# Kernel optimization log

Measured on AMD Instinct MI355X. Metric: run time of the kernel, lower is better.

The kernel has to match this reference:

```python
import jax, jax.numpy as jnp
import numpy as np

IMG = 416
NC = 80
B = 32
NOBJ = 20          # objects placed per image
K = 32             # fixed max GT boxes per image for ignore-mask IoU (>= NOBJ)
THR = 0.5
ANCHORS = np.array([[10,13],[16,30],[33,23],[30,61],[62,45],[59,119],
                    [116,90],[156,198],[373,326]], np.float32)


def _bce(logits, targets):
    # elementwise binary_cross_entropy_with_logits
    return jnp.maximum(logits, 0.0) - logits * targets + jnp.log1p(jnp.exp(-jnp.abs(logits)))


def _make_y_true(key, batch, G, nc, img, nobj):
    N = G * G * 3
    k1, k2, k3, k4 = jax.random.split(key, 4)
    idx = jax.random.randint(k1, (batch, nobj), 0, N)
    xy = jax.random.uniform(k2, (batch, nobj, 2), jnp.float32) * img
    wh = jax.random.uniform(k3, (batch, nobj, 2), jnp.float32) * 90.0 + 10.0
    cls = jax.random.randint(k4, (batch, nobj), 0, nc)
    y = jnp.zeros((batch, N, 5 + nc), jnp.float32)
    b = jnp.arange(batch)[:, None]
    y = y.at[b, idx, 0].set(xy[..., 0])
    y = y.at[b, idx, 1].set(xy[..., 1])
    y = y.at[b, idx, 2].set(wh[..., 0])
    y = y.at[b, idx, 3].set(wh[..., 1])
    y = y.at[b, idx, 4].set(1.0)
    y = y.at[b, idx, 5 + cls].set(1.0)
    return y.reshape(batch, G, G, 3, 5 + nc)


def setup_inputs() -> dict:
    key = jax.random.key(0)
    ks = jax.random.split(key, 6)
    inp = {}
    for i, G in enumerate([13, 26, 52]):
        inp[f"fm{i}"] = jax.random.normal(ks[i], (B, 3 * (5 + NC), G, G), jnp.float32)
        inp[f"yt{i}"] = _make_y_true(ks[3 + i], B, G, NC, IMG, NOBJ)
    inp["anchors"] = jnp.asarray(ANCHORS)
    return inp


def _predict_transform(fm, anchors3):
    batch, ch, G, _ = fm.shape
    A = 3
    stride = IMG // G
    bbox = 5 + NC
    # [B, A*bbox, G*G] -> [B, G*G, A*bbox] -> [B, G, G, A, bbox]
    p = fm.reshape(batch, A * bbox, G * G).transpose(0, 2, 1).reshape(batch, G, G, A, bbox)
    box_centers = jax.nn.sigmoid(p[..., 0:2])
    box_sizes_raw = p[..., 2:4]
    conf_logits = p[..., 4:5]
    prob_logits = p[..., 5:]
    ar = jnp.arange(G, dtype=fm.dtype)
    gy, gx = jnp.meshgrid(ar, ar, indexing='ij')       # row, col
    xy_offset = jnp.stack([gx, gy], axis=-1).reshape(G, G, 1, 2)
    box_centers = (box_centers + xy_offset) * stride
    box_sizes = jnp.exp(box_sizes_raw) * (anchors3 / stride) * stride
    boxes = jnp.concatenate([box_centers, box_sizes], axis=-1)
    return xy_offset, boxes, conf_logits, prob_logits


def _ignore_mask(boxes, yt):
    batch, G, _, A, _ = boxes.shape
    N = G * G * A
    pb = boxes.reshape(batch, N, 4)
    tb_all = yt[..., :4].reshape(batch, N, 4)
    obj = yt[..., 4].reshape(batch, N)
    vals, idx = jax.lax.top_k(obj, K)                  # pick up to K GT boxes
    valid = vals > 0                                    # [B,K]
    tb = jnp.take_along_axis(tb_all, idx[:, :, None], axis=1)  # [B,K,4]
    tb = jnp.where(valid[:, :, None], tb, 0.0)
    p_xy = pb[:, :, None, 0:2]; p_wh = pb[:, :, None, 2:4]     # [B,N,1,2]
    t_xy = tb[:, None, :, 0:2]; t_wh = tb[:, None, :, 2:4]     # [B,1,K,2]
    mins = jnp.maximum(p_xy - p_wh / 2.0, t_xy - t_wh / 2.0)
    maxs = jnp.minimum(p_xy + p_wh / 2.0, t_xy + t_wh / 2.0)
    iwh = jnp.maximum(maxs - mins, 0.0)
    inter = iwh[..., 0] * iwh[..., 1]                  # [B,N,K]
    p_area = p_wh[..., 0] * p_wh[..., 1]
    t_area = t_wh[..., 0] * t_wh[..., 1]
    iou = inter / (p_area + t_area - inter + 1e-10)
    iou = jnp.where(valid[:, None, :], iou, 0.0)
    best_iou = jnp.max(iou, axis=-1)                   # [B,N]
    ign = (best_iou < THR).astype(boxes.dtype)
    # original: images with no valid GT boxes keep ignore_mask = 0
    ign = jnp.where(jnp.any(valid, axis=-1)[:, None], ign, 0.0)
    return ign.reshape(batch, G, G, A, 1)


def _calculate_one(fm, yt, anchors3):
    G = fm.shape[2]
    batch = yt.shape[0]
    ratio = IMG / G
    xy_offset, boxes, conf_logits, prob_logits = _predict_transform(fm, anchors3)
    object_mask = yt[..., 4:5]
    ignore_mask = _ignore_mask(boxes, yt)
    true_xy = yt[..., 0:2] / ratio - xy_offset
    pred_xy = boxes[..., 0:2] / ratio - xy_offset
    true_tw = yt[..., 2:4] / anchors3
    pred_tw = boxes[..., 2:4] / anchors3
    true_tw = jnp.where(true_tw == 0.0, 1.0, true_tw)
    pred_tw = jnp.where(pred_tw == 0.0, 1.0, pred_tw)
    true_tw = jnp.log(jnp.clip(true_tw, 1e-9, 1e9))
    pred_tw = jnp.log(jnp.clip(pred_tw, 1e-9, 1e9))
    box_scale = 2.0 - (yt[..., 2:3] / IMG) * (yt[..., 3:4] / IMG)
    xy_loss = 5.0 * jnp.sum((true_xy - pred_xy) ** 2 * object_mask * box_scale) / batch
    wh_loss = 5.0 * jnp.sum((true_tw - pred_tw) ** 2 * object_mask * box_scale) / batch
    bce_conf = _bce(conf_logits, object_mask)
    conf_loss = object_mask * bce_conf + 0.5 * (1.0 - object_mask) * ignore_mask * bce_conf
    focal = jnp.abs(object_mask - jax.nn.sigmoid(conf_logits)) ** 2.0   # alpha=1, gamma=2
    conf_loss = jnp.sum(conf_loss * focal) / batch
    delta = 0.01
    label_target = (1.0 - delta) * yt[..., 5:] + delta / NC
    class_loss = jnp.sum(object_mask * _bce(prob_logits, label_target)) / batch
    return xy_loss, wh_loss, conf_loss, class_loss


def reference(fm0, fm1, fm2, yt0, yt1, yt2, anchors):
    anchor_groups = [anchors[6:9], anchors[3:6], anchors[0:3]]
    fms = [fm0, fm1, fm2]
    yts = [yt0, yt1, yt2]
    xy = wh = conf = prob = 0.0
    for fm, yt, a3 in zip(fms, yts, anchor_groups):
        l_xy, l_wh, l_conf, l_prob = _calculate_one(fm, yt, a3)
        xy = xy + l_xy; wh = wh + l_wh; conf = conf + l_conf; prob = prob + l_prob
    total = xy + wh + conf + prob
    return (total, xy, wh, conf, prob)
```

## Files before the change

kernel.cpp:

```cpp
#include <hip/hip_runtime.h>
#include <math.h>


constexpr int   NCLS  = 80;
constexpr int   KMAX  = 32;
constexpr float IMGF  = 416.0f;

constexpr int C0 = 32 * 3 * 169;
constexpr int C1 = 32 * 3 * 676;
constexpr int C2 = 32 * 3 * 2704;
constexpr int TOTAL_CELLS = C0 + C1 + C2;

constexpr int NBLK_POS  = 96;
constexpr int NBLK_CONF = 96 + 288 + 1056;
constexpr int NBLK_MAIN = NBLK_POS + NBLK_CONF;

constexpr size_t OFF_PART = 0;
constexpr size_t OFF_CNT  = (size_t)NBLK_MAIN * 16;
constexpr size_t OFF_TGT  = OFF_CNT + 96 * sizeof(int);
constexpr size_t OFF_TGTN = OFF_TGT + (size_t)96 * KMAX * 16;

__global__ __launch_bounds__(128) void k_init(int* cnt) {
    int t = threadIdx.x;
    if (t < 96) cnt[t] = 0;
}

__global__ __launch_bounds__(256) void k_collect(
        const float* __restrict__ yt0, const float* __restrict__ yt1,
        const float* __restrict__ yt2,
        int* __restrict__ cnt, float* __restrict__ tgt, int* __restrict__ tgtn) {
    int t = blockIdx.x * 256 + threadIdx.x;
    if (t >= TOTAL_CELLS) return;
    int s, local, G;
    const float* yt;
    if (t < C0)           { s = 0; local = t;           G = 13; yt = yt0; }
    else if (t < C0 + C1) { s = 1; local = t - C0;      G = 26; yt = yt1; }
    else                  { s = 2; local = t - C0 - C1; G = 52; yt = yt2; }
    int GG = G * G;
    int b  = local / (3 * GG);
    int n  = local - b * 3 * GG;
    int yidx = local * 85;
    float obj = yt[yidx + 4];
    if (obj > 0.5f) {
        int pos = atomicAdd(&cnt[s * 32 + b], 1);
        if (pos < KMAX) {
            float4 box = make_float4(yt[yidx], yt[yidx + 1], yt[yidx + 2], yt[yidx + 3]);
            reinterpret_cast<float4*>(tgt)[(s * 32 + b) * KMAX + pos] = box;
            tgtn[(s * 32 + b) * KMAX + pos] = n;
        }
    }
}

__device__ inline float sigmoidf_(float x) { return 1.0f / (1.0f + expf(-x)); }
__device__ inline float bcef_(float l, float t) {
    return fmaxf(l, 0.0f) - l * t + log1pf(expf(-fabsf(l)));
}

__global__ __launch_bounds__(256) void k_main(
        const float* __restrict__ fm0, const float* __restrict__ fm1,
        const float* __restrict__ fm2,
        const float* __restrict__ yt0, const float* __restrict__ yt1,
        const float* __restrict__ yt2,
        const float* __restrict__ anch,
        const int* __restrict__ cnt, const float* __restrict__ tgt,
        const int* __restrict__ tgtn, float4* __restrict__ part) {
    __shared__ float s_minx[KMAX], s_maxx[KMAX], s_miny[KMAX], s_maxy[KMAX], s_area[KMAX];
    __shared__ int   s_tn[KMAX];
    __shared__ int   s_cn;
    __shared__ float4 s_w4[4];
    __shared__ float  s_w1[4];

    int bid = blockIdx.x;
    int tid = threadIdx.x;
    int wid = tid >> 6, lane = tid & 63;

    if (bid < NBLK_POS) {
        int sb = bid, s = sb >> 5, b = sb & 31;
        const float *fm, *yt;
        int G, anchoff;
        if (s == 0)      { fm = fm0; yt = yt0; G = 13; anchoff = 6; }
        else if (s == 1) { fm = fm1; yt = yt1; G = 26; anchoff = 3; }
        else             { fm = fm2; yt = yt2; G = 52; anchoff = 0; }
        int GG = G * G;
        float stridef = IMGF / (float)G;
        int cn = min(cnt[sb], KMAX);
        float accx = 0.f, accw = 0.f, accp = 0.f;
        for (int slot = wid; slot < cn; slot += 4) {
            float4 tb = reinterpret_cast<const float4*>(tgt)[sb * KMAX + slot];
            int n  = tgtn[sb * KMAX + slot];
            int a  = n % 3;
            int sp = n / 3;
            int jj = sp % G, ii = sp / G;
            int ybase = (b * 3 * GG + n) * 85;
            int fbase = (b * 255 + a * 85) * GG + sp;
            float ps = 0.0f;
            for (int c = lane; c < NCLS; c += 64) {
                float pl  = fm[fbase + (5 + c) * GG];
                float tl  = yt[ybase + 5 + c];
                float lab = 0.99f * tl + 1.25e-4f;
                ps += bcef_(pl, lab);
            }
            for (int off = 32; off; off >>= 1) ps += __shfl_down(ps, off);
            if (lane == 0) {
                float p0 = fm[fbase];
                float p1 = fm[fbase + GG];
                float p2 = fm[fbase + 2 * GG];
                float p3 = fm[fbase + 3 * GG];
                float bcx = (sigmoidf_(p0) + (float)jj) * stridef;
                float bcy = (sigmoidf_(p1) + (float)ii) * stridef;
                float predx = bcx / stridef - (float)jj;
                float predy = bcy / stridef - (float)ii;
                float truex = tb.x / stridef - (float)jj;
                float truey = tb.y / stridef - (float)ii;
                float dx = truex - predx, dy = truey - predy;
                float bscale = 2.0f - (tb.z / IMGF) * (tb.w / IMGF);
                float aw = anch[(anchoff + a) * 2], ah = anch[(anchoff + a) * 2 + 1];
                float pw = expf(p2) * (aw / stridef) * stridef;
                float ph = expf(p3) * (ah / stridef) * stridef;
                float ptw = pw / aw, pth = ph / ah;
                float ttw = tb.z / aw, tth = tb.w / ah;
                ttw = (ttw == 0.0f) ? 1.0f : ttw;
                tth = (tth == 0.0f) ? 1.0f : tth;
                ptw = (ptw == 0.0f) ? 1.0f : ptw;
                pth = (pth == 0.0f) ? 1.0f : pth;
                ttw = logf(fminf(fmaxf(ttw, 1e-9f), 1e9f));
                tth = logf(fminf(fmaxf(tth, 1e-9f), 1e9f));
                ptw = logf(fminf(fmaxf(ptw, 1e-9f), 1e9f));
                pth = logf(fminf(fmaxf(pth, 1e-9f), 1e9f));
                float dw = ttw - ptw, dh = tth - pth;
                accx += (dx * dx + dy * dy) * bscale;
                accw += (dw * dw + dh * dh) * bscale;
                accp += ps;
            }
        }
        if (lane == 0) s_w4[wid] = make_float4(accx, accw, accp, 0.f);
        __syncthreads();
        if (tid == 0) {
            float4 r0 = s_w4[0], r1 = s_w4[1], r2 = s_w4[2], r3 = s_w4[3];
            part[bid] = make_float4(r0.x + r1.x + r2.x + r3.x,
                                    r0.y + r1.y + r2.y + r3.y,
                                    r0.z + r1.z + r2.z + r3.z,
                                    0.0f);
        }
    } else {
        int cb = bid - NBLK_POS;
        const float *fm;
        int G, chunks, s, anchoff;
        if (cb < 96)       { fm = fm0; G = 13; chunks = 1;  s = 0; anchoff = 6; }
        else if (cb < 384) { cb -= 96;  fm = fm1; G = 26; chunks = 3;  s = 1; anchoff = 3; }
        else               { cb -= 384; fm = fm2; G = 52; chunks = 11; s = 2; anchoff = 0; }
        int chunk = cb % chunks;
        int ba    = cb / chunks;
        int b = ba / 3, a = ba % 3;
        int GG = G * G;
        float stridef = IMGF / (float)G;
        int sb = s * 32 + b;

        if (tid == 0) s_cn = min(cnt[sb], KMAX);
        if (tid < KMAX) {
            float4 tb = reinterpret_cast<const float4*>(tgt)[sb * KMAX + tid];
            s_minx[tid] = tb.x - tb.z * 0.5f;
            s_maxx[tid] = tb.x + tb.z * 0.5f;
            s_miny[tid] = tb.y - tb.w * 0.5f;
            s_maxy[tid] = tb.y + tb.w * 0.5f;
            s_area[tid] = tb.z * tb.w;
            s_tn[tid]   = tgtn[sb * KMAX + tid];
        }
        __syncthreads();

        int sp = chunk * 256 + tid;
        float local = 0.0f;
        if (sp < GG) {
            int jj = sp % G, ii = sp / G;
            int n = sp * 3 + a;
            int fbase = (b * 255 + a * 85) * GG + sp;
            float p0 = fm[fbase];
            float p1 = fm[fbase + GG];
            float p2 = fm[fbase + 2 * GG];
            float p3 = fm[fbase + 3 * GG];
            float p4 = fm[fbase + 4 * GG];
            float aw = anch[(anchoff + a) * 2], ah = anch[(anchoff + a) * 2 + 1];
            float cx = (sigmoidf_(p0) + (float)jj) * stridef;
            float cy = (sigmoidf_(p1) + (float)ii) * stridef;
            float pw = expf(p2) * (aw / stridef) * stridef;
            float ph = expf(p3) * (ah / stridef) * stridef;
            float pminx = cx - pw * 0.5f, pmaxx = cx + pw * 0.5f;
            float pminy = cy - ph * 0.5f, pmaxy = cy + ph * 0.5f;
            float parea = pw * ph;
            int cn = s_cn;
            float best = 0.0f;
            float m = 0.0f;
            for (int k = 0; k < cn; ++k) {
                if (s_tn[k] == n) m = 1.0f;
                float iw = fminf(pmaxx, s_maxx[k]) - fmaxf(pminx, s_minx[k]);
                float ih = fminf(pmaxy, s_maxy[k]) - fmaxf(pminy, s_miny[k]);
                iw = fmaxf(iw, 0.0f);
                ih = fmaxf(ih, 0.0f);
                float inter = iw * ih;
                float iou = inter / ((parea + s_area[k] - inter) + 1e-10f);
                best = fmaxf(best, iou);
            }
            float ign = (cn > 0 && best < 0.5f) ? 1.0f : 0.0f;
            float bce = bcef_(p4, m);
            float d = fabsf(m - sigmoidf_(p4));
            local = (m * bce + 0.5f * (1.0f - m) * ign * bce) * (d * d);
        }
        for (int off = 32; off; off >>= 1) local += __shfl_down(local, off);
        if (lane == 0) s_w1[wid] = local;
        __syncthreads();
        if (tid == 0)
            part[bid] = make_float4(0.f, 0.f, 0.f, s_w1[0] + s_w1[1] + s_w1[2] + s_w1[3]);
    }
}

__global__ __launch_bounds__(512) void k_reduce(
        const float4* __restrict__ part, float* __restrict__ out) {
    int t = threadIdx.x;
    double x = 0.0, w = 0.0, p = 0.0, c = 0.0;
    for (int i = t; i < NBLK_MAIN; i += 512) {
        float4 v = part[i];
        x += (double)v.x; w += (double)v.y; p += (double)v.z; c += (double)v.w;
    }
    for (int off = 32; off; off >>= 1) {
        x += __shfl_down(x, off);
        w += __shfl_down(w, off);
        p += __shfl_down(p, off);
        c += __shfl_down(c, off);
    }
    __shared__ double sx[8], sw[8], sp[8], sc[8];
    int wid = t >> 6, lane = t & 63;
    if (lane == 0) { sx[wid] = x; sw[wid] = w; sp[wid] = p; sc[wid] = c; }
    __syncthreads();
    if (t == 0) {
        double X = 0, W = 0, P = 0, C = 0;
        for (int i = 0; i < 8; ++i) { X += sx[i]; W += sw[i]; P += sp[i]; C += sc[i]; }
        double xy = 5.0 * X / 32.0;
        double wh = 5.0 * W / 32.0;
        double cf = C / 32.0;
        double pb = P / 32.0;
        out[0] = (float)(xy + wh + cf + pb);
        out[1] = (float)xy;
        out[2] = (float)wh;
        out[3] = (float)cf;
        out[4] = (float)pb;
    }
}

extern "C" void kernel_launch(void* const* d_in, const int* in_sizes, int n_in,
                              void* d_out, int out_size, void* d_ws, size_t ws_size,
                              hipStream_t stream) {
    const float* fm0  = (const float*)d_in[0];
    const float* yt0  = (const float*)d_in[1];
    const float* fm1  = (const float*)d_in[2];
    const float* yt1  = (const float*)d_in[3];
    const float* fm2  = (const float*)d_in[4];
    const float* yt2  = (const float*)d_in[5];
    const float* anch = (const float*)d_in[6];
    float* out = (float*)d_out;

    char* ws = (char*)d_ws;
    float4* part = (float4*)(ws + OFF_PART);
    int*    cnt  = (int*)(ws + OFF_CNT);
    float*  tgt  = (float*)(ws + OFF_TGT);
    int*    tgtn = (int*)(ws + OFF_TGTN);

    k_init<<<1, 128, 0, stream>>>(cnt);
    k_collect<<<(TOTAL_CELLS + 255) / 256, 256, 0, stream>>>(
        yt0, yt1, yt2, cnt, tgt, tgtn);
    k_main<<<NBLK_MAIN, 256, 0, stream>>>(
        fm0, fm1, fm2, yt0, yt1, yt2, anch, cnt, tgt, tgtn, part);
    k_reduce<<<1, 512, 0, stream>>>(part, out);
}
```

Baseline: 41.55 us.

## Fuse collect, loss and reduce into one persistent kernel with grid barrier

Merges the collect, main and reduce kernels into a single persistent kernel of 512 blocks. A software grid barrier (atomic counter with spin-wait) separates target collection from loss computation, and the last block to finish does the final reduction. It also sorts each image's targets by cell index so the class-loss summation order is deterministic. This removes two kernel launches and their gaps, but adds a spin barrier that relies on all 512 blocks being resident at once, and reduces parallelism in the collect phase.

```diff
diff --git a/kernel.cpp b/kernel.cpp
--- a/kernel.cpp
+++ b/kernel.cpp
@@ -11,238 +11,278 @@
 constexpr int C2 = 32 * 3 * 2704;
 constexpr int TOTAL_CELLS = C0 + C1 + C2;
 
-constexpr int NBLK_POS  = 96;
-constexpr int NBLK_CONF = 96 + 288 + 1056;
-constexpr int NBLK_MAIN = NBLK_POS + NBLK_CONF;
-
-constexpr size_t OFF_PART = 0;
-constexpr size_t OFF_CNT  = (size_t)NBLK_MAIN * 16;
-constexpr size_t OFF_TGT  = OFF_CNT + 96 * sizeof(int);
-constexpr size_t OFF_TGTN = OFF_TGT + (size_t)96 * KMAX * 16;
-
-__global__ __launch_bounds__(128) void k_init(int* cnt) {
-    int t = threadIdx.x;
-    if (t < 96) cnt[t] = 0;
-}
-
-__global__ __launch_bounds__(256) void k_collect(
-        const float* __restrict__ yt0, const float* __restrict__ yt1,
-        const float* __restrict__ yt2,
-        int* __restrict__ cnt, float* __restrict__ tgt, int* __restrict__ tgtn) {
-    int t = blockIdx.x * 256 + threadIdx.x;
-    if (t >= TOTAL_CELLS) return;
-    int s, local, G;
-    const float* yt;
-    if (t < C0)           { s = 0; local = t;           G = 13; yt = yt0; }
-    else if (t < C0 + C1) { s = 1; local = t - C0;      G = 26; yt = yt1; }
-    else                  { s = 2; local = t - C0 - C1; G = 52; yt = yt2; }
-    int GG = G * G;
-    int b  = local / (3 * GG);
-    int n  = local - b * 3 * GG;
-    int yidx = local * 85;
-    float obj = yt[yidx + 4];
-    if (obj > 0.5f) {
-        int pos = atomicAdd(&cnt[s * 32 + b], 1);
-        if (pos < KMAX) {
-            float4 box = make_float4(yt[yidx], yt[yidx + 1], yt[yidx + 2], yt[yidx + 3]);
-            reinterpret_cast<float4*>(tgt)[(s * 32 + b) * KMAX + pos] = box;
-            tgtn[(s * 32 + b) * KMAX + pos] = n;
-        }
-    }
-}
-
+constexpr int NBLK  = 512;
+constexpr int NUNIT = 96 + 1440;
+
+constexpr size_t OFF_CNT   = 0;
+constexpr size_t OFF_DONE1 = 384;
+constexpr size_t OFF_DONE2 = 448;
+constexpr size_t OFF_PART  = 512;
+constexpr size_t OFF_TGT   = OFF_PART + (size_t)NBLK * 16;
+constexpr size_t OFF_TGTN  = OFF_TGT + (size_t)96 * KMAX * 16;
+
+__device__ __forceinline__ int aload_i(const int* p) {
+    return __hip_atomic_load(p, __ATOMIC_RELAXED, __HIP_MEMORY_SCOPE_AGENT);
+}
+__device__ __forceinline__ float aload_f(const float* p) {
+    return __hip_atomic_load(p, __ATOMIC_RELAXED, __HIP_MEMORY_SCOPE_AGENT);
+}
 __device__ inline float sigmoidf_(float x) { return 1.0f / (1.0f + expf(-x)); }
 __device__ inline float bcef_(float l, float t) {
     return fmaxf(l, 0.0f) - l * t + log1pf(expf(-fabsf(l)));
 }
 
-__global__ __launch_bounds__(256) void k_main(
+__global__ __launch_bounds__(128) void k_init(int* wsi) {
+    int t = threadIdx.x;
+    if (t < 128) wsi[t] = 0;
+}
+
+__global__ __launch_bounds__(256, 2) void k_mega(
         const float* __restrict__ fm0, const float* __restrict__ fm1,
         const float* __restrict__ fm2,
         const float* __restrict__ yt0, const float* __restrict__ yt1,
         const float* __restrict__ yt2,
         const float* __restrict__ anch,
-        const int* __restrict__ cnt, const float* __restrict__ tgt,
-        const int* __restrict__ tgtn, float4* __restrict__ part) {
-    __shared__ float s_minx[KMAX], s_maxx[KMAX], s_miny[KMAX], s_maxy[KMAX], s_area[KMAX];
-    __shared__ int   s_tn[KMAX];
-    __shared__ int   s_cn;
-    __shared__ float4 s_w4[4];
-    __shared__ float  s_w1[4];
+        int* __restrict__ cnt, float* __restrict__ tgt, int* __restrict__ tgtn,
+        int* __restrict__ done1, int* __restrict__ done2,
+        float* __restrict__ part, float* __restrict__ out) {
+    __shared__ float4 s_t4[KMAX];
+    __shared__ float  s_minx[KMAX], s_maxx[KMAX], s_miny[KMAX], s_maxy[KMAX], s_area[KMAX];
+    __shared__ int    s_tn[KMAX];
+    __shared__ int    s_cn;
+    __shared__ float4 s_w[4];
+    __shared__ int    s_last;
 
     int bid = blockIdx.x;
     int tid = threadIdx.x;
     int wid = tid >> 6, lane = tid & 63;
 
-    if (bid < NBLK_POS) {
-        int sb = bid, s = sb >> 5, b = sb & 31;
-        const float *fm, *yt;
-        int G, anchoff;
-        if (s == 0)      { fm = fm0; yt = yt0; G = 13; anchoff = 6; }
-        else if (s == 1) { fm = fm1; yt = yt1; G = 26; anchoff = 3; }
-        else             { fm = fm2; yt = yt2; G = 52; anchoff = 0; }
+    for (int t = bid * 256 + tid; t < TOTAL_CELLS; t += NBLK * 256) {
+        int s, local, G;
+        const float* yt;
+        if (t < C0)           { s = 0; local = t;           G = 13; yt = yt0; }
+        else if (t < C0 + C1) { s = 1; local = t - C0;      G = 26; yt = yt1; }
+        else                  { s = 2; local = t - C0 - C1; G = 52; yt = yt2; }
         int GG = G * G;
-        float stridef = IMGF / (float)G;
-        int cn = min(cnt[sb], KMAX);
-        float accx = 0.f, accw = 0.f, accp = 0.f;
-        for (int slot = wid; slot < cn; slot += 4) {
-            float4 tb = reinterpret_cast<const float4*>(tgt)[sb * KMAX + slot];
-            int n  = tgtn[sb * KMAX + slot];
-            int a  = n % 3;
-            int sp = n / 3;
-            int jj = sp % G, ii = sp / G;
-            int ybase = (b * 3 * GG + n) * 85;
-            int fbase = (b * 255 + a * 85) * GG + sp;
-            float ps = 0.0f;
-            for (int c = lane; c < NCLS; c += 64) {
-                float pl  = fm[fbase + (5 + c) * GG];
-                float tl  = yt[ybase + 5 + c];
-                float lab = 0.99f * tl + 1.25e-4f;
-                ps += bcef_(pl, lab);
-            }
-            for (int off = 32; off; off >>= 1) ps += __shfl_down(ps, off);
-            if (lane == 0) {
+        int b  = local / (3 * GG);
+        int n  = local - b * 3 * GG;
+        int yidx = local * 85;
+        float obj = yt[yidx + 4];
+        if (obj > 0.5f) {
+            int pos = atomicAdd(&cnt[s * 32 + b], 1);
+            if (pos < KMAX) {
+                float4 box = make_float4(yt[yidx], yt[yidx + 1], yt[yidx + 2], yt[yidx + 3]);
+                reinterpret_cast<float4*>(tgt)[(s * 32 + b) * KMAX + pos] = box;
+                tgtn[(s * 32 + b) * KMAX + pos] = n;
+            }
+        }
+    }
+    __syncthreads();
+    if (tid == 0) {
+        __threadfence();
+        atomicAdd(done1, 1);
+        while (__hip_atomic_load(done1, __ATOMIC_ACQUIRE, __HIP_MEMORY_SCOPE_AGENT) < NBLK)
+            __builtin_amdgcn_s_sleep(2);
+    }
+    __syncthreads();
+
+    float ax = 0.f, aw2 = 0.f, ap = 0.f, ac = 0.f;
+
+    for (int unit = bid; unit < NUNIT; unit += NBLK) {
+        __syncthreads();
+        if (unit < 96) {
+            int sb = unit, s = sb >> 5, b = sb & 31;
+            const float *fm, *yt;
+            int G, anchoff;
+            if (s == 0)      { fm = fm0; yt = yt0; G = 13; anchoff = 6; }
+            else if (s == 1) { fm = fm1; yt = yt1; G = 26; anchoff = 3; }
+            else             { fm = fm2; yt = yt2; G = 52; anchoff = 0; }
+            int GG = G * G;
+            float stridef = IMGF / (float)G;
+            if (tid == 0) s_cn = min(aload_i(&cnt[sb]), KMAX);
+            if (tid < KMAX) {
+                const float* tp = tgt + (size_t)(sb * KMAX + tid) * 4;
+                s_t4[tid] = make_float4(aload_f(tp), aload_f(tp + 1),
+                                        aload_f(tp + 2), aload_f(tp + 3));
+                s_tn[tid] = aload_i(&tgtn[sb * KMAX + tid]);
+            }
+            __syncthreads();
+            if (tid == 0) {
+                int cn = s_cn;
+                for (int i = 1; i < cn; ++i) {
+                    int key = s_tn[i]; float4 kv = s_t4[i];
+                    int j = i - 1;
+                    while (j >= 0 && s_tn[j] > key) {
+                        s_tn[j + 1] = s_tn[j]; s_t4[j + 1] = s_t4[j]; --j;
+                    }
+                    s_tn[j + 1] = key; s_t4[j + 1] = kv;
+                }
+            }
+            __syncthreads();
+            int cn = s_cn;
+            for (int slot = wid; slot < cn; slot += 4) {
+                float4 tb = s_t4[slot];
+                int n  = s_tn[slot];
+                int a  = n % 3;
+                int sp = n / 3;
+                int jj = sp % G, ii = sp / G;
+                int ybase = (b * 3 * GG + n) * 85;
+                int fbase = (b * 255 + a * 85) * GG + sp;
+                for (int c = lane; c < NCLS; c += 64) {
+                    float pl  = fm[fbase + (5 + c) * GG];
+                    float tl  = yt[ybase + 5 + c];
+                    float lab = 0.99f * tl + 1.25e-4f;
+                    ap += bcef_(pl, lab);
+                }
+                if (lane == 0) {
+                    float p0 = fm[fbase];
+                    float p1 = fm[fbase + GG];
+                    float p2 = fm[fbase + 2 * GG];
+                    float p3 = fm[fbase + 3 * GG];
+                    float bcx = (sigmoidf_(p0) + (float)jj) * stridef;
+                    float bcy = (sigmoidf_(p1) + (float)ii) * stridef;
+                    float predx = bcx / stridef - (float)jj;
+                    float predy = bcy / stridef - (float)ii;
+                    float truex = tb.x / stridef - (float)jj;
+                    float truey = tb.y / stridef - (float)ii;
+                    float dx = truex - predx, dy = truey - predy;
+                    float bscale = 2.0f - (tb.z / IMGF) * (tb.w / IMGF);
+                    float aw = anch[(anchoff + a) * 2], ah = anch[(anchoff + a) * 2 + 1];
+                    float pw = expf(p2) * (aw / stridef) * stridef;
+                    float ph = expf(p3) * (ah / stridef) * stridef;
+                    float ptw = pw / aw, pth = ph / ah;
+                    float ttw = tb.z / aw, tth = tb.w / ah;
+                    ttw = (ttw == 0.0f) ? 1.0f : ttw;
+                    tth = (tth == 0.0f) ? 1.0f : tth;
+                    ptw = (ptw == 0.0f) ? 1.0f : ptw;
+                    pth = (pth == 0.0f) ? 1.0f : pth;
+                    ttw = logf(fminf(fmaxf(ttw, 1e-9f), 1e9f));
+                    tth = logf(fminf(fmaxf(tth, 1e-9f), 1e9f));
+                    ptw = logf(fminf(fmaxf(ptw, 1e-9f), 1e9f));
+                    pth = logf(fminf(fmaxf(pth, 1e-9f), 1e9f));
+                    float dw = ttw - ptw, dh = tth - pth;
+                    ax  += (dx * dx + dy * dy) * bscale;
+                    aw2 += (dw * dw + dh * dh) * bscale;
+                }
+            }
+        } else {
+            int cb = unit - 96;
+            const float *fm;
+            int G, chunks, s, anchoff;
+            if (cb < 96)       { fm = fm0; G = 13; chunks = 1;  s = 0; anchoff = 6; }
+            else if (cb < 384) { cb -= 96;  fm = fm1; G = 26; chunks = 3;  s = 1; anchoff = 3; }
+            else               { cb -= 384; fm = fm2; G = 52; chunks = 11; s = 2; anchoff = 0; }
+            int chunk = cb % chunks;
+            int ba    = cb / chunks;
+            int b = ba / 3, a = ba % 3;
+            int GG = G * G;
+            float stridef = IMGF / (float)G;
+            int sb = s * 32 + b;
+            if (tid == 0) s_cn = min(aload_i(&cnt[sb]), KMAX);
+            if (tid < KMAX) {
+                const float* tp = tgt + (size_t)(sb * KMAX + tid) * 4;
+                float x = aload_f(tp), y = aload_f(tp + 1);
+                float w = aload_f(tp + 2), h = aload_f(tp + 3);
+                s_minx[tid] = x - w * 0.5f;
+                s_maxx[tid] = x + w * 0.5f;
+                s_miny[tid] = y - h * 0.5f;
+                s_maxy[tid] = y + h * 0.5f;
+                s_area[tid] = w * h;
+                s_tn[tid]   = aload_i(&tgtn[sb * KMAX + tid]);
+            }
+            __syncthreads();
+            int sp = chunk * 256 + tid;
+            if (sp < GG) {
+                int jj = sp % G, ii = sp / G;
+                int n = sp * 3 + a;
+                int fbase = (b * 255 + a * 85) * GG + sp;
                 float p0 = fm[fbase];
                 float p1 = fm[fbase + GG];
                 float p2 = fm[fbase + 2 * GG];
                 float p3 = fm[fbase + 3 * GG];
-                float bcx = (sigmoidf_(p0) + (float)jj) * stridef;
-                float bcy = (sigmoidf_(p1) + (float)ii) * stridef;
-                float predx = bcx / stridef - (float)jj;
-                float predy = bcy / stridef - (float)ii;
-                float truex = tb.x / stridef - (float)jj;
-                float truey = tb.y / stridef - (float)ii;
-                float dx = truex - predx, dy = truey - predy;
-                float bscale = 2.0f - (tb.z / IMGF) * (tb.w / IMGF);
+                float p4 = fm[fbase + 4 * GG];
                 float aw = anch[(anchoff + a) * 2], ah = anch[(anchoff + a) * 2 + 1];
+                float cx = (sigmoidf_(p0) + (float)jj) * stridef;
+                float cy = (sigmoidf_(p1) + (float)ii) * stridef;
                 float pw = expf(p2) * (aw / stridef) * stridef;
                 float ph = expf(p3) * (ah / stridef) * stridef;
-                float ptw = pw / aw, pth = ph / ah;
-                float ttw = tb.z / aw, tth = tb.w / ah;
-                ttw = (ttw == 0.0f) ? 1.0f : ttw;
-                tth = (tth == 0.0f) ? 1.0f : tth;
-                ptw = (ptw == 0.0f) ? 1.0f : ptw;
-                pth = (pth == 0.0f) ? 1.0f : pth;
-                ttw = logf(fminf(fmaxf(ttw, 1e-9f), 1e9f));
-                tth = logf(fminf(fmaxf(tth, 1e-9f), 1e9f));
-                ptw = logf(fminf(fmaxf(ptw, 1e-9f), 1e9f));
-                pth = logf(fminf(fmaxf(pth, 1e-9f), 1e9f));
-                float dw = ttw - ptw, dh = tth - pth;
-                accx += (dx * dx + dy * dy) * bscale;
-                accw += (dw * dw + dh * dh) * bscale;
-                accp += ps;
-            }
-        }
-        if (lane == 0) s_w4[wid] = make_float4(accx, accw, accp, 0.f);
+                float pminx = cx - pw * 0.5f, pmaxx = cx + pw * 0.5f;
+                float pminy = cy - ph * 0.5f, pmaxy = cy + ph * 0.5f;
+                float parea = pw * ph;
+                int cn = s_cn;
+                float best = 0.0f, m = 0.0f;
+                for (int k = 0; k < cn; ++k) {
+                    if (s_tn[k] == n) m = 1.0f;
+                    float iw = fminf(pmaxx, s_maxx[k]) - fmaxf(pminx, s_minx[k]);
+                    float ih = fminf(pmaxy, s_maxy[k]) - fmaxf(pminy, s_miny[k]);
+                    iw = fmaxf(iw, 0.0f);
+                    ih = fmaxf(ih, 0.0f);
+                    float inter = iw * ih;
+                    float iou = inter / ((parea + s_area[k] - inter) + 1e-10f);
+                    best = fmaxf(best, iou);
+                }
+                float ign = (cn > 0 && best < 0.5f) ? 1.0f : 0.0f;
+                float bce = bcef_(p4, m);
+                float d = fabsf(m - sigmoidf_(p4));
+                ac += (m * bce + 0.5f * (1.0f - m) * ign * bce) * (d * d);
+            }
+        }
+    }
+
+    for (int off = 32; off; off >>= 1) {
+        ax  += __shfl_down(ax,  off);
+        aw2 += __shfl_down(aw2, off);
+        ap  += __shfl_down(ap,  off);
+        ac  += __shfl_down(ac,  off);
+    }
+    if (lane == 0) s_w[wid] = make_float4(ax, aw2, ap, ac);
+    __syncthreads();
+    if (tid == 0) {
+        float4 r0 = s_w[0], r1 = s_w[1], r2 = s_w[2], r3 = s_w[3];
+        float4 v = make_float4(r0.x + r1.x + r2.x + r3.x,
+                               r0.y + r1.y + r2.y + r3.y,
+                               r0.z + r1.z + r2.z + r3.z,
+                               r0.w + r1.w + r2.w + r3.w);
+        reinterpret_cast<float4*>(part)[bid] = v;
+        __threadfence();
+        int prev = atomicAdd(done2, 1);
+        s_last = (prev == NBLK - 1) ? 1 : 0;
+    }
+    __syncthreads();
+
+    if (s_last) {
+        double dx = 0.0, dw = 0.0, dp = 0.0, dc = 0.0;
+        for (int i = tid; i < NBLK; i += 256) {
+            const float* pp = part + (size_t)i * 4;
+            dx += (double)aload_f(pp);
+            dw += (double)aload_f(pp + 1);
+            dp += (double)aload_f(pp + 2);
+            dc += (double)aload_f(pp + 3);
+        }
+        for (int off = 32; off; off >>= 1) {
+            dx += __shfl_down(dx, off);
+            dw += __shfl_down(dw, off);
+            dp += __shfl_down(dp, off);
+            dc += __shfl_down(dc, off);
+        }
+        __shared__ double sd[4][4];
+        if (lane == 0) { sd[wid][0] = dx; sd[wid][1] = dw; sd[wid][2] = dp; sd[wid][3] = dc; }
         __syncthreads();
         if (tid == 0) {
-            float4 r0 = s_w4[0], r1 = s_w4[1], r2 = s_w4[2], r3 = s_w4[3];
-            part[bid] = make_float4(r0.x + r1.x + r2.x + r3.x,
-                                    r0.y + r1.y + r2.y + r3.y,
-                                    r0.z + r1.z + r2.z + r3.z,
-                                    0.0f);
-        }
-    } else {
-        int cb = bid - NBLK_POS;
-        const float *fm;
-        int G, chunks, s, anchoff;
-        if (cb < 96)       { fm = fm0; G = 13; chunks = 1;  s = 0; anchoff = 6; }
-        else if (cb < 384) { cb -= 96;  fm = fm1; G = 26; chunks = 3;  s = 1; anchoff = 3; }
-        else               { cb -= 384; fm = fm2; G = 52; chunks = 11; s = 2; anchoff = 0; }
-        int chunk = cb % chunks;
-        int ba    = cb / chunks;
-        int b = ba / 3, a = ba % 3;
-        int GG = G * G;
-        float stridef = IMGF / (float)G;
-        int sb = s * 32 + b;
-
-        if (tid == 0) s_cn = min(cnt[sb], KMAX);
-        if (tid < KMAX) {
-            float4 tb = reinterpret_cast<const float4*>(tgt)[sb * KMAX + tid];
-            s_minx[tid] = tb.x - tb.z * 0.5f;
-            s_maxx[tid] = tb.x + tb.z * 0.5f;
-            s_miny[tid] = tb.y - tb.w * 0.5f;
-            s_maxy[tid] = tb.y + tb.w * 0.5f;
-            s_area[tid] = tb.z * tb.w;
-            s_tn[tid]   = tgtn[sb * KMAX + tid];
-        }
-        __syncthreads();
-
-        int sp = chunk * 256 + tid;
-        float local = 0.0f;
-        if (sp < GG) {
-            int jj = sp % G, ii = sp / G;
-            int n = sp * 3 + a;
-            int fbase = (b * 255 + a * 85) * GG + sp;
-            float p0 = fm[fbase];
-            float p1 = fm[fbase + GG];
-            float p2 = fm[fbase + 2 * GG];
-            float p3 = fm[fbase + 3 * GG];
-            float p4 = fm[fbase + 4 * GG];
-            float aw = anch[(anchoff + a) * 2], ah = anch[(anchoff + a) * 2 + 1];
-            float cx = (sigmoidf_(p0) + (float)jj) * stridef;
-            float cy = (sigmoidf_(p1) + (float)ii) * stridef;
-            float pw = expf(p2) * (aw / stridef) * stridef;
-            float ph = expf(p3) * (ah / stridef) * stridef;
-            float pminx = cx - pw * 0.5f, pmaxx = cx + pw * 0.5f;
-            float pminy = cy - ph * 0.5f, pmaxy = cy + ph * 0.5f;
-            float parea = pw * ph;
-            int cn = s_cn;
-            float best = 0.0f;
-            float m = 0.0f;
-            for (int k = 0; k < cn; ++k) {
-                if (s_tn[k] == n) m = 1.0f;
-                float iw = fminf(pmaxx, s_maxx[k]) - fmaxf(pminx, s_minx[k]);
-                float ih = fminf(pmaxy, s_maxy[k]) - fmaxf(pminy, s_miny[k]);
-                iw = fmaxf(iw, 0.0f);
-                ih = fmaxf(ih, 0.0f);
-                float inter = iw * ih;
-                float iou = inter / ((parea + s_area[k] - inter) + 1e-10f);
-                best = fmaxf(best, iou);
-            }
-            float ign = (cn > 0 && best < 0.5f) ? 1.0f : 0.0f;
-            float bce = bcef_(p4, m);
-            float d = fabsf(m - sigmoidf_(p4));
-            local = (m * bce + 0.5f * (1.0f - m) * ign * bce) * (d * d);
-        }
-        for (int off = 32; off; off >>= 1) local += __shfl_down(local, off);
-        if (lane == 0) s_w1[wid] = local;
-        __syncthreads();
-        if (tid == 0)
-            part[bid] = make_float4(0.f, 0.f, 0.f, s_w1[0] + s_w1[1] + s_w1[2] + s_w1[3]);
-    }
-}
-
-__global__ __launch_bounds__(512) void k_reduce(
-        const float4* __restrict__ part, float* __restrict__ out) {
-    int t = threadIdx.x;
-    double x = 0.0, w = 0.0, p = 0.0, c = 0.0;
-    for (int i = t; i < NBLK_MAIN; i += 512) {
-        float4 v = part[i];
-        x += (double)v.x; w += (double)v.y; p += (double)v.z; c += (double)v.w;
-    }
-    for (int off = 32; off; off >>= 1) {
-        x += __shfl_down(x, off);
-        w += __shfl_down(w, off);
-        p += __shfl_down(p, off);
-        c += __shfl_down(c, off);
-    }
-    __shared__ double sx[8], sw[8], sp[8], sc[8];
-    int wid = t >> 6, lane = t & 63;
-    if (lane == 0) { sx[wid] = x; sw[wid] = w; sp[wid] = p; sc[wid] = c; }
-    __syncthreads();
-    if (t == 0) {
-        double X = 0, W = 0, P = 0, C = 0;
-        for (int i = 0; i < 8; ++i) { X += sx[i]; W += sw[i]; P += sp[i]; C += sc[i]; }
-        double xy = 5.0 * X / 32.0;
-        double wh = 5.0 * W / 32.0;
-        double cf = C / 32.0;
-        double pb = P / 32.0;
-        out[0] = (float)(xy + wh + cf + pb);
-        out[1] = (float)xy;
-        out[2] = (float)wh;
-        out[3] = (float)cf;
-        out[4] = (float)pb;
+            double X = sd[0][0] + sd[1][0] + sd[2][0] + sd[3][0];
+            double W = sd[0][1] + sd[1][1] + sd[2][1] + sd[3][1];
+            double P = sd[0][2] + sd[1][2] + sd[2][2] + sd[3][2];
+            double C = sd[0][3] + sd[1][3] + sd[2][3] + sd[3][3];
+            double xy = 5.0 * X / 32.0;
+            double wh = 5.0 * W / 32.0;
+            double cf = C / 32.0;
+            double pb = P / 32.0;
+            out[0] = (float)(xy + wh + cf + pb);
+            out[1] = (float)xy;
+            out[2] = (float)wh;
+            out[3] = (float)cf;
+            out[4] = (float)pb;
+        }
     }
 }
 
@@ -259,15 +299,15 @@
     float* out = (float*)d_out;
 
     char* ws = (char*)d_ws;
-    float4* part = (float4*)(ws + OFF_PART);
-    int*    cnt  = (int*)(ws + OFF_CNT);
-    float*  tgt  = (float*)(ws + OFF_TGT);
-    int*    tgtn = (int*)(ws + OFF_TGTN);
-
-    k_init<<<1, 128, 0, stream>>>(cnt);
-    k_collect<<<(TOTAL_CELLS + 255) / 256, 256, 0, stream>>>(
-        yt0, yt1, yt2, cnt, tgt, tgtn);
-    k_main<<<NBLK_MAIN, 256, 0, stream>>>(
-        fm0, fm1, fm2, yt0, yt1, yt2, anch, cnt, tgt, tgtn, part);
-    k_reduce<<<1, 512, 0, stream>>>(part, out);
-}
+    int*   cnt   = (int*)(ws + OFF_CNT);
+    int*   done1 = (int*)(ws + OFF_DONE1);
+    int*   done2 = (int*)(ws + OFF_DONE2);
+    float* part  = (float*)(ws + OFF_PART);
+    float* tgt   = (float*)(ws + OFF_TGT);
+    int*   tgtn  = (int*)(ws + OFF_TGTN);
+
+    k_init<<<1, 128, 0, stream>>>((int*)ws);
+    k_mega<<<NBLK, 256, 0, stream>>>(
+        fm0, fm1, fm2, yt0, yt1, yt2, anch,
+        cnt, tgt, tgtn, done1, done2, part, out);
+}
```

Measured after the change: 123.3 us. 197% more time.

## Replace atomic target collection with partitioned ballot compaction and spread positive work

Applied to the files above, without the earlier changes.

The init kernel and the atomic-based per-cell collect are replaced by one collect kernel in which each block scans a partition of one image's cells and compacts positives with wave ballots and prefix counts. This removes a launch and the atomics, and gives a deterministic slot order. The positive-box part of the main kernel now gives each wave one target slot across 768 blocks, where before one block looped over all targets of an image. All partial sums go through one shared four-way reduction. The cost is more main-kernel blocks that mostly exit at once, and conf blocks that load 128 shared target entries instead of 32.

```diff
diff --git a/kernel.cpp b/kernel.cpp
--- a/kernel.cpp
+++ b/kernel.cpp
@@ -3,57 +3,83 @@
 
 
 constexpr int   NCLS  = 80;
-constexpr int   KMAX  = 32;
+constexpr int   PMAX  = 4;
+constexpr int   SLOTS = 32;
 constexpr float IMGF  = 416.0f;
 
-constexpr int C0 = 32 * 3 * 169;
-constexpr int C1 = 32 * 3 * 676;
-constexpr int C2 = 32 * 3 * 2704;
-constexpr int TOTAL_CELLS = C0 + C1 + C2;
-
-constexpr int NBLK_POS  = 96;
+constexpr int NBLK_COLLECT = 32 * (1 + 2 + 4);
+constexpr int NBLK_POS  = 768;
 constexpr int NBLK_CONF = 96 + 288 + 1056;
 constexpr int NBLK_MAIN = NBLK_POS + NBLK_CONF;
 
-constexpr size_t OFF_PART = 0;
-constexpr size_t OFF_CNT  = (size_t)NBLK_MAIN * 16;
-constexpr size_t OFF_TGT  = OFF_CNT + 96 * sizeof(int);
-constexpr size_t OFF_TGTN = OFF_TGT + (size_t)96 * KMAX * 16;
-
-__global__ __launch_bounds__(128) void k_init(int* cnt) {
-    int t = threadIdx.x;
-    if (t < 96) cnt[t] = 0;
-}
-
-__global__ __launch_bounds__(256) void k_collect(
+constexpr size_t OFF_CNT  = 0;
+constexpr size_t OFF_PART = 1536;
+constexpr size_t OFF_TGT  = OFF_PART + (size_t)NBLK_MAIN * 16;
+constexpr size_t OFF_TGTN = OFF_TGT + (size_t)96 * PMAX * SLOTS * 16;
+
+__device__ inline float sigmoidf_(float x) { return 1.0f / (1.0f + expf(-x)); }
+__device__ inline float bcef_(float l, float t) {
+    return fmaxf(l, 0.0f) - l * t + log1pf(expf(-fabsf(l)));
+}
+
+__global__ __launch_bounds__(512) void k_collect(
         const float* __restrict__ yt0, const float* __restrict__ yt1,
         const float* __restrict__ yt2,
         int* __restrict__ cnt, float* __restrict__ tgt, int* __restrict__ tgtn) {
-    int t = blockIdx.x * 256 + threadIdx.x;
-    if (t >= TOTAL_CELLS) return;
-    int s, local, G;
+    int bid = blockIdx.x, tid = threadIdx.x;
+    int lane = tid & 63, wid = tid >> 6;
+    int s, b, p, P, G;
     const float* yt;
-    if (t < C0)           { s = 0; local = t;           G = 13; yt = yt0; }
-    else if (t < C0 + C1) { s = 1; local = t - C0;      G = 26; yt = yt1; }
-    else                  { s = 2; local = t - C0 - C1; G = 52; yt = yt2; }
-    int GG = G * G;
-    int b  = local / (3 * GG);
-    int n  = local - b * 3 * GG;
-    int yidx = local * 85;
-    float obj = yt[yidx + 4];
-    if (obj > 0.5f) {
-        int pos = atomicAdd(&cnt[s * 32 + b], 1);
-        if (pos < KMAX) {
-            float4 box = make_float4(yt[yidx], yt[yidx + 1], yt[yidx + 2], yt[yidx + 3]);
-            reinterpret_cast<float4*>(tgt)[(s * 32 + b) * KMAX + pos] = box;
-            tgtn[(s * 32 + b) * KMAX + pos] = n;
+    if (bid < 32)      { s = 0; b = bid;            p = 0;       P = 1; yt = yt0; G = 13; }
+    else if (bid < 96) { s = 1; int i = bid - 32; b = i >> 1; p = i & 1; P = 2; yt = yt1; G = 26; }
+    else               { s = 2; int i = bid - 96; b = i >> 2; p = i & 3; P = 4; yt = yt2; G = 52; }
+    int GG3  = 3 * G * G;
+    int per  = (GG3 + P - 1) / P;
+    int nbase = p * per;
+    int count = min(per, GG3 - nbase);
+    int nit  = (count + 511) / 512;
+    int sb = s * 32 + b;
+
+    __shared__ int s_wcnt[8];
+    __shared__ int s_base;
+    if (tid == 0) s_base = 0;
+
+    float obj[4];
+    int   nn[4];
+    #pragma unroll
+    for (int it = 0; it < 4; ++it) {
+        int c = it * 512 + tid;
+        nn[it]  = nbase + c;
+        obj[it] = 0.0f;
+        if (c < count) obj[it] = yt[(size_t)(b * GG3 + nn[it]) * 85 + 4];
+    }
+    __syncthreads();
+
+    for (int it = 0; it < nit; ++it) {
+        bool pos = obj[it] > 0.5f;
+        unsigned long long mask = __ballot(pos);
+        if (lane == 0) s_wcnt[wid] = __popcll(mask);
+        __syncthreads();
+        int wpre = 0, tot = 0;
+        #pragma unroll
+        for (int w = 0; w < 8; ++w) { if (w < wid) wpre += s_wcnt[w]; tot += s_wcnt[w]; }
+        int rank = s_base + wpre + (int)__popcll(mask & ((1ull << lane) - 1ull));
+        if (pos && rank < SLOTS) {
+            size_t yb = (size_t)(b * GG3 + nn[it]) * 85;
+            int slot = (sb * PMAX + p) * SLOTS + rank;
+            float4 box = make_float4(yt[yb], yt[yb + 1], yt[yb + 2], yt[yb + 3]);
+            reinterpret_cast<float4*>(tgt)[slot] = box;
+            tgtn[slot] = nn[it];
         }
-    }
-}
-
-__device__ inline float sigmoidf_(float x) { return 1.0f / (1.0f + expf(-x)); }
-__device__ inline float bcef_(float l, float t) {
-    return fmaxf(l, 0.0f) - l * t + log1pf(expf(-fabsf(l)));
+        __syncthreads();
+        if (tid == 0) s_base += tot;
+        __syncthreads();
+    }
+    if (tid == 0) {
+        cnt[sb * PMAX + p] = min(s_base, SLOTS);
+        if (p == 0)
+            for (int q = P; q < PMAX; ++q) cnt[sb * PMAX + q] = 0;
+    }
 }
 
 __global__ __launch_bounds__(256) void k_main(
@@ -64,43 +90,50 @@
         const float* __restrict__ anch,
         const int* __restrict__ cnt, const float* __restrict__ tgt,
         const int* __restrict__ tgtn, float4* __restrict__ part) {
-    __shared__ float s_minx[KMAX], s_maxx[KMAX], s_miny[KMAX], s_maxy[KMAX], s_area[KMAX];
-    __shared__ int   s_tn[KMAX];
-    __shared__ int   s_cn;
-    __shared__ float4 s_w4[4];
-    __shared__ float  s_w1[4];
+    __shared__ float  s_minx[128], s_maxx[128], s_miny[128], s_maxy[128], s_area[128];
+    __shared__ int    s_tn[128];
+    __shared__ int    s_cn4[4];
+    __shared__ float4 s_w[4];
 
     int bid = blockIdx.x;
     int tid = threadIdx.x;
     int wid = tid >> 6, lane = tid & 63;
 
+    float ax = 0.f, aw2 = 0.f, ap = 0.f, ac = 0.f;
+
     if (bid < NBLK_POS) {
-        int sb = bid, s = sb >> 5, b = sb & 31;
+        int slot = bid * 4 + wid;
+        int sb = slot >> 5, idx = slot & 31;
+        int s = sb >> 5, b = sb & 31;
         const float *fm, *yt;
         int G, anchoff;
         if (s == 0)      { fm = fm0; yt = yt0; G = 13; anchoff = 6; }
         else if (s == 1) { fm = fm1; yt = yt1; G = 26; anchoff = 3; }
         else             { fm = fm2; yt = yt2; G = 52; anchoff = 0; }
-        int GG = G * G;
-        float stridef = IMGF / (float)G;
-        int cn = min(cnt[sb], KMAX);
-        float accx = 0.f, accw = 0.f, accp = 0.f;
-        for (int slot = wid; slot < cn; slot += 4) {
-            float4 tb = reinterpret_cast<const float4*>(tgt)[sb * KMAX + slot];
-            int n  = tgtn[sb * KMAX + slot];
+        int c0 = cnt[sb * PMAX + 0], c1 = cnt[sb * PMAX + 1];
+        int c2 = cnt[sb * PMAX + 2], c3 = cnt[sb * PMAX + 3];
+        int cn_total = c0 + c1 + c2 + c3;
+        if (idx < cn_total) {
+            int p = 0, rem = idx;
+            if (rem >= c0) { rem -= c0; p = 1;
+                if (rem >= c1) { rem -= c1; p = 2;
+                    if (rem >= c2) { rem -= c2; p = 3; } } }
+            int entry = (sb * PMAX + p) * SLOTS + rem;
+            int GG = G * G;
+            float stridef = IMGF / (float)G;
+            float4 tb = reinterpret_cast<const float4*>(tgt)[entry];
+            int n  = tgtn[entry];
             int a  = n % 3;
             int sp = n / 3;
             int jj = sp % G, ii = sp / G;
             int ybase = (b * 3 * GG + n) * 85;
             int fbase = (b * 255 + a * 85) * GG + sp;
-            float ps = 0.0f;
             for (int c = lane; c < NCLS; c += 64) {
                 float pl  = fm[fbase + (5 + c) * GG];
                 float tl  = yt[ybase + 5 + c];
                 float lab = 0.99f * tl + 1.25e-4f;
-                ps += bcef_(pl, lab);
+                ap += bcef_(pl, lab);
             }
-            for (int off = 32; off; off >>= 1) ps += __shfl_down(ps, off);
             if (lane == 0) {
                 float p0 = fm[fbase];
                 float p1 = fm[fbase + GG];
@@ -128,19 +161,9 @@
                 ptw = logf(fminf(fmaxf(ptw, 1e-9f), 1e9f));
                 pth = logf(fminf(fmaxf(pth, 1e-9f), 1e9f));
                 float dw = ttw - ptw, dh = tth - pth;
-                accx += (dx * dx + dy * dy) * bscale;
-                accw += (dw * dw + dh * dh) * bscale;
-                accp += ps;
+                ax  += (dx * dx + dy * dy) * bscale;
+                aw2 += (dw * dw + dh * dh) * bscale;
             }
-        }
-        if (lane == 0) s_w4[wid] = make_float4(accx, accw, accp, 0.f);
-        __syncthreads();
-        if (tid == 0) {
-            float4 r0 = s_w4[0], r1 = s_w4[1], r2 = s_w4[2], r3 = s_w4[3];
-            part[bid] = make_float4(r0.x + r1.x + r2.x + r3.x,
-                                    r0.y + r1.y + r2.y + r3.y,
-                                    r0.z + r1.z + r2.z + r3.z,
-                                    0.0f);
         }
     } else {
         int cb = bid - NBLK_POS;
@@ -155,21 +178,19 @@
         int GG = G * G;
         float stridef = IMGF / (float)G;
         int sb = s * 32 + b;
-
-        if (tid == 0) s_cn = min(cnt[sb], KMAX);
-        if (tid < KMAX) {
-            float4 tb = reinterpret_cast<const float4*>(tgt)[sb * KMAX + tid];
+        if (tid < 4) s_cn4[tid] = cnt[sb * PMAX + tid];
+        if (tid < 128) {
+            int slot = sb * PMAX * SLOTS + tid;
+            float4 tb = reinterpret_cast<const float4*>(tgt)[slot];
             s_minx[tid] = tb.x - tb.z * 0.5f;
             s_maxx[tid] = tb.x + tb.z * 0.5f;
             s_miny[tid] = tb.y - tb.w * 0.5f;
             s_maxy[tid] = tb.y + tb.w * 0.5f;
             s_area[tid] = tb.z * tb.w;
-            s_tn[tid]   = tgtn[sb * KMAX + tid];
+            s_tn[tid]   = tgtn[slot];
         }
         __syncthreads();
-
         int sp = chunk * 256 + tid;
-        float local = 0.0f;
         if (sp < GG) {
             int jj = sp % G, ii = sp / G;
             int n = sp * 3 + a;
@@ -187,29 +208,45 @@
             float pminx = cx - pw * 0.5f, pmaxx = cx + pw * 0.5f;
             float pminy = cy - ph * 0.5f, pmaxy = cy + ph * 0.5f;
             float parea = pw * ph;
-            int cn = s_cn;
-            float best = 0.0f;
-            float m = 0.0f;
-            for (int k = 0; k < cn; ++k) {
-                if (s_tn[k] == n) m = 1.0f;
-                float iw = fminf(pmaxx, s_maxx[k]) - fmaxf(pminx, s_minx[k]);
-                float ih = fminf(pmaxy, s_maxy[k]) - fmaxf(pminy, s_miny[k]);
-                iw = fmaxf(iw, 0.0f);
-                ih = fmaxf(ih, 0.0f);
-                float inter = iw * ih;
-                float iou = inter / ((parea + s_area[k] - inter) + 1e-10f);
-                best = fmaxf(best, iou);
+            float best = 0.0f, m = 0.0f;
+            int cn_total = 0;
+            #pragma unroll
+            for (int p = 0; p < PMAX; ++p) {
+                int cnp = s_cn4[p];
+                cn_total += cnp;
+                for (int k = 0; k < cnp; ++k) {
+                    int e = p * SLOTS + k;
+                    if (s_tn[e] == n) m = 1.0f;
+                    float iw = fminf(pmaxx, s_maxx[e]) - fmaxf(pminx, s_minx[e]);
+                    float ih = fminf(pmaxy, s_maxy[e]) - fmaxf(pminy, s_miny[e]);
+                    iw = fmaxf(iw, 0.0f);
+                    ih = fmaxf(ih, 0.0f);
+                    float inter = iw * ih;
+                    float iou = inter / ((parea + s_area[e] - inter) + 1e-10f);
+                    best = fmaxf(best, iou);
+                }
             }
-            float ign = (cn > 0 && best < 0.5f) ? 1.0f : 0.0f;
+            float ign = (cn_total > 0 && best < 0.5f) ? 1.0f : 0.0f;
             float bce = bcef_(p4, m);
             float d = fabsf(m - sigmoidf_(p4));
-            local = (m * bce + 0.5f * (1.0f - m) * ign * bce) * (d * d);
+            ac += (m * bce + 0.5f * (1.0f - m) * ign * bce) * (d * d);
         }
-        for (int off = 32; off; off >>= 1) local += __shfl_down(local, off);
-        if (lane == 0) s_w1[wid] = local;
-        __syncthreads();
-        if (tid == 0)
-            part[bid] = make_float4(0.f, 0.f, 0.f, s_w1[0] + s_w1[1] + s_w1[2] + s_w1[3]);
+    }
+
+    for (int off = 32; off; off >>= 1) {
+        ax  += __shfl_down(ax,  off);
+        aw2 += __shfl_down(aw2, off);
+        ap  += __shfl_down(ap,  off);
+        ac  += __shfl_down(ac,  off);
+    }
+    if (lane == 0) s_w[wid] = make_float4(ax, aw2, ap, ac);
+    __syncthreads();
+    if (tid == 0) {
+        float4 r0 = s_w[0], r1 = s_w[1], r2 = s_w[2], r3 = s_w[3];
+        part[bid] = make_float4(r0.x + r1.x + r2.x + r3.x,
+                                r0.y + r1.y + r2.y + r3.y,
+                                r0.z + r1.z + r2.z + r3.z,
+                                r0.w + r1.w + r2.w + r3.w);
     }
 }
 
@@ -259,14 +296,12 @@
     float* out = (float*)d_out;
 
     char* ws = (char*)d_ws;
+    int*    cnt  = (int*)(ws + OFF_CNT);
     float4* part = (float4*)(ws + OFF_PART);
-    int*    cnt  = (int*)(ws + OFF_CNT);
     float*  tgt  = (float*)(ws + OFF_TGT);
     int*    tgtn = (int*)(ws + OFF_TGTN);
 
-    k_init<<<1, 128, 0, stream>>>(cnt);
-    k_collect<<<(TOTAL_CELLS + 255) / 256, 256, 0, stream>>>(
-        yt0, yt1, yt2, cnt, tgt, tgtn);
+    k_collect<<<NBLK_COLLECT, 512, 0, stream>>>(yt0, yt1, yt2, cnt, tgt, tgtn);
     k_main<<<NBLK_MAIN, 256, 0, stream>>>(
         fm0, fm1, fm2, yt0, yt1, yt2, anch, cnt, tgt, tgtn, part);
     k_reduce<<<1, 512, 0, stream>>>(part, out);
```

Result: faster. 35.40 us (-14.8%).
